# Performance work log

Hardware: AMD Instinct MI355X
Metric: run time of the kernel (lower is better)

The kernel has to match this reference:

```python
import jax, jax.numpy as jnp
import numpy as np
from jax import lax

# Module hyperparameters (init_kwargs)
B, T, F, H = 512, 256, 64, 128
D = F + H            # decoder LSTMCell width = input_dim + hidden_rnn
OUT_DIM = 32         # output_dim (survival horizon steps)
RISKS = 2
NEG = -1e10


def lstm_cell(x, h, c, Wih, Whh):
    # PyTorch gate order: i, f, g, o; bias=False
    g = x @ Wih.T + h @ Whh.T
    i, f, gg, o = jnp.split(g, 4, axis=-1)
    c = jax.nn.sigmoid(f) * c + jax.nn.sigmoid(i) * jnp.tanh(gg)
    h = jax.nn.sigmoid(o) * jnp.tanh(c)
    return h, c


def setup_inputs() -> dict:
    key = jax.random.key(0)
    ks = jax.random.split(key, 12)
    rn = lambda k, shp, fan: jax.random.normal(k, shp, jnp.float32) * (1.0 / np.sqrt(fan))
    return {
        "x": jax.random.normal(ks[0], (B, T, F), jnp.float32),
        # encoder LSTM (1 layer, bias=False)
        "W_ih_emb": rn(ks[1], (4 * H, F), F),
        "W_hh_emb": rn(ks[2], (4 * H, H), H),
        # longitudinal head: Linear(H -> F)
        "W_long": rn(ks[3], (F, H), H),
        "b_long": jnp.zeros((F,), jnp.float32),
        # attention head: Linear(F+H -> 1)
        "W_att": rn(ks[4], (1, D), D),
        "b_att": jnp.zeros((1,), jnp.float32),
        # per-risk cause-specific LSTMCell (bias=False) and Linear(D -> 1)
        "W_ih_cs": rn(ks[5], (RISKS, 4 * D, D), D),
        "W_hh_cs": rn(ks[6], (RISKS, 4 * D, D), D),
        "W_cs": rn(ks[7], (RISKS, 1, D), D),
        "b_cs": jnp.zeros((RISKS, 1), jnp.float32),
    }


def _forward(x, W_ih_emb, W_hh_emb, W_long, b_long, W_att, b_att,
             W_ih_cs, W_hh_cs, W_cs, b_cs):
    inputmask = jnp.abs(x).sum(2) == 0                      # [B,T]
    last_obs = (~inputmask).sum(axis=1) - 1                 # [B]

    # encoder LSTM over time
    def enc_step(carry, xt):
        h, c = carry
        h, c = lstm_cell(xt, h, c, W_ih_emb, W_hh_emb)
        return (h, c), h

    h0 = jnp.zeros((x.shape[0], H), x.dtype)
    _, hs = lax.scan(enc_step, (h0, h0), x.transpose(1, 0, 2))
    hidden = hs.transpose(1, 0, 2)                          # [B,T,H]

    long_pred = hidden @ W_long.T + b_long                  # [B,T,F]

    x_last = x[jnp.arange(x.shape[0]), last_obs]            # [B,F]
    concat = jnp.concatenate(
        [hidden, jnp.broadcast_to(x_last[:, None, :], (x.shape[0], x.shape[1], F))], -1)
    scores = (concat @ W_att.T + b_att)[..., 0]             # [B,T]

    idx = jnp.arange(x.shape[1])[None, :]
    scores = jnp.where(idx >= last_obs[:, None], NEG, scores)
    att = jax.nn.softmax(scores, axis=1)
    att = jnp.where((last_obs > 0)[:, None], att, 0.0)      # rows with last_obs==0 zeroed

    hidden_att = jnp.einsum('bt,bth->bh', att, hidden)      # [B,H]
    ha = jnp.concatenate([hidden_att, x_last], 1)           # [B,D]

    state0 = (lax.stop_gradient(ha), lax.stop_gradient(ha))  # .detach() on init state
    rs = jnp.arange(OUT_DIM * RISKS) % RISKS                # k-major, r-minor loop order

    def dec_step(carry, r):
        h, c = carry
        h, c = lstm_cell(ha, h, c, W_ih_cs[r], W_hh_cs[r])
        out = jax.nn.sigmoid(h @ W_cs[r].T + b_cs[r])       # [B,1]
        return (h, c), out

    _, outs = lax.scan(dec_step, state0, rs)                # [steps,B,1]
    outcomes = jax.nn.softmax(outs[..., 0].T, axis=-1)      # [B, OUT_DIM*RISKS]
    parts = tuple(outcomes[:, i * OUT_DIM:(i + 1) * OUT_DIM] for i in range(RISKS))
    return (long_pred,) + parts


def reference(x, W_ih_emb, W_hh_emb, W_long, b_long, W_att, b_att,
              W_ih_cs, W_hh_cs, W_cs, b_cs):
    return _forward(x, W_ih_emb, W_hh_emb, W_long, b_long, W_att, b_att,
                    W_ih_cs, W_hh_cs, W_cs, b_cs)
```

## Files before the change

kernel.cpp:

```cpp
#include <hip/hip_runtime.h>
#include <stdint.h>

#define DEV __device__ __forceinline__
typedef unsigned short u16; typedef unsigned int u32; typedef unsigned long long u64;
typedef __attribute__((ext_vector_type(8))) short s8v;
typedef __attribute__((ext_vector_type(4))) float f4v;

#define Bb 512
#define Tt 256
#define Ff 64
#define Hh 128
#define Dd 192

DEV u16 f2bf(float f){ u32 u = __builtin_bit_cast(u32, f); u32 r = (u + 0x7fffu + ((u>>16)&1u)) >> 16; return (u16)r; }
DEV float bf2f(u16 h){ u32 u = ((u32)h)<<16; return __builtin_bit_cast(float, u); }
DEV float sigm(float x){ return __builtin_amdgcn_rcpf(1.0f + __expf(-x)); }
DEV float tanhfast(float x){ return 1.0f - 2.0f*__builtin_amdgcn_rcpf(1.0f + __expf(2.0f*x)); }

DEV f4v mfma16(s8v a, s8v b, f4v c){ return __builtin_amdgcn_mfma_f32_16x16x32_bf16(a, b, c, 0, 0, 0); }

DEV void barrier_lds(){ asm volatile("s_waitcnt lgkmcnt(0)\n\ts_barrier" ::: "memory"); }

DEV int hxe(int k, int c){ int blk = k>>3; return (blk*16 + (c ^ ((blk&3)<<1)))*8 + (k&7); }

DEV s8v pack8(const float* p){
  const float4 a = *(const float4*)p; const float4 b = *(const float4*)(p+4);
  s8v r; r[0]=(short)f2bf(a.x); r[1]=(short)f2bf(a.y); r[2]=(short)f2bf(a.z); r[3]=(short)f2bf(a.w);
  r[4]=(short)f2bf(b.x); r[5]=(short)f2bf(b.y); r[6]=(short)f2bf(b.z); r[7]=(short)f2bf(b.w); return r;
}
DEV u32 pk2(float a, float b){ return (u32)f2bf(a) | ((u32)f2bf(b)<<16); }

__global__ __launch_bounds__(64) void prelim_k(const float* __restrict__ x,
    const float* __restrict__ Watt, const float* __restrict__ batt,
    float* __restrict__ xlast, float* __restrict__ c0, int* __restrict__ lastobs)
{
  int b = blockIdx.x, tid = threadIdx.x;
  int cnt = 0;
  for (int it = 0; it < 4; ++it){
    int t = it*64 + tid;
    const float4* p = (const float4*)(x + ((size_t)b*Tt + t)*Ff);
    float s = 0.0f;
    #pragma unroll
    for (int q = 0; q < 16; ++q){ float4 v = p[q]; s += fabsf(v.x)+fabsf(v.y)+fabsf(v.z)+fabsf(v.w); }
    u64 m = __ballot(s != 0.0f);
    cnt += __popcll(m);
  }
  int last = cnt - 1;
  int li = (last < 0) ? (Tt-1) : last;
  float xl = x[((size_t)b*Tt + li)*Ff + tid];
  xlast[b*Ff + tid] = xl;
  float p = xl * Watt[Hh + tid];
  for (int off = 32; off; off >>= 1) p += __shfl_down(p, off);
  if (tid == 0){ c0[b] = p + batt[0]; lastobs[b] = last; }
}

__global__ __launch_bounds__(256) void prep_wd_k(const float* __restrict__ Whhcs,
    const float* __restrict__ Wihcs, u16* __restrict__ Wd, u16* __restrict__ WdIH)
{
  int idx = blockIdx.x*256 + threadIdx.x;
  int j = idx & 7, lane = (idx>>3)&63;
  int f = idx>>9;
  int kt = f % 6; int mtr = f/6;
  int mt = mtr % 48, r = mtr/48;
  int ut = mt>>2, g = mt&3;
  int row = g*Dd + ut*16 + (lane&15);
  int k = kt*32 + (lane>>4)*8 + j;
  size_t src = ((size_t)r*768 + row)*Dd + k;
  Wd[idx]   = f2bf(Whhcs[src]);
  WdIH[idx] = f2bf(Wihcs[src]);
}

__global__ __launch_bounds__(64) void xw_k(const u16* __restrict__ WdIH,
    const float* __restrict__ ha, u16* __restrict__ xwg)
{
  int lane = threadIdx.x, l15 = lane&15, l4 = lane>>4;
  int cg = blockIdx.x & 3, rm = blockIdx.x >> 2;
  s8v af[6];
  #pragma unroll
  for (int kt=0;kt<6;++kt) af[kt] = *(const s8v*)(WdIH + (size_t)(rm*6+kt)*512 + lane*8);
  #pragma unroll
  for (int ct=0; ct<8; ++ct){
    int c = cg*128 + ct*16 + l15;
    f4v a = {0,0,0,0};
    #pragma unroll
    for (int kt=0;kt<6;++kt){
      s8v b = pack8(ha + (size_t)c*Dd + kt*32 + l4*8);
      a = mfma16(af[kt], b, a);
    }
    int bg = cg*8 + ct;
    int base = bg*24576 + rm*256 + l15*16 + l4*4;
    *(u32*)&xwg[base]   = pk2(a[0], a[1]);
    *(u32*)&xwg[base+2] = pk2(a[2], a[3]);
  }
}

__global__ __launch_bounds__(512,2) void enc_k(
    const float* __restrict__ x, const float* __restrict__ Whh, const float* __restrict__ Wih,
    const float* __restrict__ Wlong, const float* __restrict__ blong, const float* __restrict__ Watt,
    const float* __restrict__ xlast, const float* __restrict__ c0v, const int* __restrict__ lastobs,
    float* __restrict__ lp_out, float* __restrict__ ha)
{
  __shared__ __align__(16) u16 hx[2][3072];
  __shared__ float lp_lds[2][16*68];
  __shared__ float sarr[2][16];
  const int tid = threadIdx.x, wid = tid>>6, lane = tid&63, l15 = lane&15, l4 = lane>>4;
  const int b0 = blockIdx.x*16;
  const int xrow = tid>>5, xc2 = (tid&31)*2;

  s8v wf[4][6];
  #pragma unroll
  for (int mt = 0; mt < 4; ++mt){
    int gate = mt*Hh + wid*16 + l15;
    #pragma unroll
    for (int kt = 0; kt < 6; ++kt){
      int k0 = kt*32 + l4*8;
      if (kt < 4) wf[mt][kt] = pack8(Whh + (size_t)gate*Hh + k0);
      else        wf[mt][kt] = pack8(Wih + (size_t)gate*Ff + (k0 - Hh));
    }
  }
  s8v wfx[6];
  {
    s8v z = {0,0,0,0,0,0,0,0};
    #pragma unroll
    for (int kt = 0; kt < 6; ++kt) wfx[kt] = z;
    if (wid < 4){
      int f = wid*16 + l15;
      #pragma unroll
      for (int kt = 0; kt < 4; ++kt) wfx[kt] = pack8(Wlong + (size_t)f*Hh + kt*32 + l4*8);
    } else if (wid == 4 && l15 == 0){
      #pragma unroll
      for (int kt = 0; kt < 4; ++kt) wfx[kt] = pack8(Watt + kt*32 + l4*8);
    }
  }
  float bl[4] = {0,0,0,0};
  if (wid < 4){
    #pragma unroll
    for (int j = 0; j < 4; ++j) bl[j] = blong[wid*16 + l4*4 + j];
  }
  const int   lastb = lastobs[b0 + l15];
  const float c0b   = c0v[b0 + l15];

  const int he0 = hxe(wid*16 + l4*4, l15);
  const int xe0 = hxe(Hh + xc2, xrow);

  ((u64*)hx[0])[tid] = 0ull;
  {
    float2 xv = *(const float2*)(x + ((size_t)(b0+xrow)*Tt + 0)*Ff + xc2);
    *(u32*)&hx[0][xe0] = pk2(xv.x, xv.y);
  }
  float2 xa[4], xb[4];
  #pragma unroll
  for (int u = 0; u < 4; ++u)
    xa[u] = *(const float2*)(x + ((size_t)(b0+xrow)*Tt + (1+u))*Ff + xc2);
  __syncthreads();

  float cst[4] = {0,0,0,0}, hp[4] = {0,0,0,0}, hpp[4] = {0,0,0,0};
  float accA[4] = {0,0,0,0}, mrun = -3.0e38f, zrun = 0.0f;

  for (int tb = 0; tb < Tt; tb += 4){
    #pragma unroll
    for (int u = 0; u < 4; ++u){
      int tp = tb + 5 + u; if (tp > Tt-1) tp = Tt-1;
      xb[u] = *(const float2*)(x + ((size_t)(b0+xrow)*Tt + tp)*Ff + xc2);
    }
    #pragma unroll
    for (int u = 0; u < 4; ++u){
      const int t = tb + u;
      const int curb = u & 1, nxtb = curb ^ 1;
      s8v bf[6];
      #pragma unroll
      for (int kt = 0; kt < 6; ++kt)
        bf[kt] = *(const s8v*)&hx[curb][((kt*4 + l4)*16 + (l15 ^ (l4<<1)))*8];

      f4v acc0 = {0,0,0,0}, acc1 = {0,0,0,0}, acc2 = {0,0,0,0}, acc3 = {0,0,0,0}, accx = {0,0,0,0};
      #pragma unroll
      for (int kt = 0; kt < 6; ++kt){
        acc0 = mfma16(wf[0][kt], bf[kt], acc0);
        acc1 = mfma16(wf[1][kt], bf[kt], acc1);
        acc2 = mfma16(wf[2][kt], bf[kt], acc2);
        acc3 = mfma16(wf[3][kt], bf[kt], acc3);
      }
      if (wid < 5){
        #pragma unroll
        for (int kt = 0; kt < 6; ++kt) accx = mfma16(wfx[kt], bf[kt], accx);
      }
      if (wid == 4 && l4 == 0) sarr[nxtb][l15] = accx[0] + c0b;

      float hnew[4];
      #pragma unroll
      for (int j = 0; j < 4; ++j){
        float cn = sigm(acc1[j])*cst[j] + sigm(acc0[j])*tanhfast(acc2[j]);
        cst[j] = cn;
        hnew[j] = sigm(acc3[j])*tanhfast(cn);
      }
      if (t >= 2){
        float sv = sarr[curb][l15];
        if (t-2 < lastb){
          float mn = fmaxf(mrun, sv);
          float sc = __expf(mrun - mn);
          float e  = __expf(sv - mn);
          zrun = zrun*sc + e;
          #pragma unroll
          for (int j = 0; j < 4; ++j) accA[j] = accA[j]*sc + e*hpp[j];
          mrun = mn;
        }
      }
      #pragma unroll
      for (int j = 0; j < 4; ++j){ hpp[j] = hp[j]; hp[j] = hnew[j]; }
      {
        u64 w = (u64)pk2(hnew[0],hnew[1]) | ((u64)pk2(hnew[2],hnew[3])<<32);
        *(u64*)&hx[nxtb][he0] = w;
      }
      if (t < Tt-1) *(u32*)&hx[nxtb][xe0] = pk2(xa[u].x, xa[u].y);
      if (wid < 4){
        #pragma unroll
        for (int j = 0; j < 4; ++j)
          lp_lds[nxtb][l15*68 + wid*16 + l4*4 + j] = accx[j] + bl[j];
      }
      if (t >= 2){
        float2 v; v.x = lp_lds[curb][xrow*68 + xc2]; v.y = lp_lds[curb][xrow*68 + xc2 + 1];
        *(float2*)(lp_out + ((size_t)(b0+xrow)*Tt + (t-2))*Ff + xc2) = v;
      }
      barrier_lds();
    }
    #pragma unroll
    for (int u = 0; u < 4; ++u) xa[u] = xb[u];
  }
  {
    if (254 < lastb){
      float sv = sarr[0][l15];
      float mn = fmaxf(mrun, sv);
      float sc = __expf(mrun - mn);
      float e  = __expf(sv - mn);
      zrun = zrun*sc + e;
      #pragma unroll
      for (int j = 0; j < 4; ++j) accA[j] = accA[j]*sc + e*hpp[j];
      mrun = mn;
    }
    { float2 v; v.x = lp_lds[0][xrow*68 + xc2]; v.y = lp_lds[0][xrow*68 + xc2 + 1];
      *(float2*)(lp_out + ((size_t)(b0+xrow)*Tt + 254)*Ff + xc2) = v; }
    s8v bfE[4];
    #pragma unroll
    for (int kt = 0; kt < 4; ++kt)
      bfE[kt] = *(const s8v*)&hx[0][((kt*4 + l4)*16 + (l15 ^ (l4<<1)))*8];
    if (wid < 4){
      f4v accx = {0,0,0,0};
      #pragma unroll
      for (int kt = 0; kt < 4; ++kt) accx = mfma16(wfx[kt], bfE[kt], accx);
      #pragma unroll
      for (int j = 0; j < 4; ++j) lp_lds[1][l15*68 + wid*16 + l4*4 + j] = accx[j] + bl[j];
    }
    float inv = (zrun > 0.0f) ? __builtin_amdgcn_rcpf(zrun) : 0.0f;
    #pragma unroll
    for (int j = 0; j < 4; ++j)
      ha[(size_t)(b0 + l15)*Dd + wid*16 + l4*4 + j] = accA[j]*inv;
    __syncthreads();
    { float2 v; v.x = lp_lds[1][xrow*68 + xc2]; v.y = lp_lds[1][xrow*68 + xc2 + 1];
      *(float2*)(lp_out + ((size_t)(b0+xrow)*Tt + 255)*Ff + xc2) = v; }
    for (int q = tid; q < 16*Ff; q += 512){
      int r2 = q >> 6, f = q & 63;
      ha[(size_t)(b0 + r2)*Dd + Hh + f] = xlast[(b0 + r2)*Ff + f];
    }
  }
}

__global__ __launch_bounds__(256,1) void dec_k(const float* __restrict__ ha,
    const u16* __restrict__ Wd, const u16* __restrict__ xwg,
    const float* __restrict__ Wcs, const float* __restrict__ bcs, float* __restrict__ outs)
{
  __shared__ __align__(16) u16 hx[2][3072];
  __shared__ __align__(16) u16 w1[48*2*512];
  __shared__ __align__(16) u16 xwl[2*48*256];
  __shared__ float red[2][4][16];
  const int tid = threadIdx.x, wid = tid>>6, lane = tid&63, l15 = lane&15, l4 = lane>>4;
  const int b0 = blockIdx.x*16;

  #pragma unroll
  for (int it = 0; it < 3; ++it){
    int k = it*64 + (tid>>4)*4, c = tid&15;
    float4 v = *(const float4*)(ha + (size_t)(b0+c)*Dd + k);
    int e = hxe(k, c);
    *(u32*)&hx[0][e]   = pk2(v.x, v.y);
    *(u32*)&hx[0][e+2] = pk2(v.z, v.w);
  }
  {
    const u16* src = xwg + (size_t)blockIdx.x*24576;
    #pragma unroll
    for (int i = 0; i < 12; ++i){
      int off = (i*256 + tid)*8;
      *(s8v*)&xwl[off] = *(const s8v*)(src + off);
    }
  }
  #pragma unroll
  for (int i = 0; i < 24; ++i){
    int off = (i*256 + tid)*8;
    int chunk = off>>9, inner = off&511;
    int mtg = chunk>>1, kt = chunk&1;
    *(s8v*)&w1[off] = *(const s8v*)(Wd + (size_t)((48+mtg)*6+kt)*512 + inner);
  }
  s8v wreg[12][6];
  #pragma unroll
  for (int m = 0; m < 12; ++m)
    #pragma unroll
    for (int kt = 0; kt < 6; ++kt)
      wreg[m][kt] = *(const s8v*)(Wd + (size_t)((wid*12+m)*6+kt)*512 + lane*8);

  float cst[3][4], wcsr0[3][4], wcsr1[3][4];
  #pragma unroll
  for (int ut = 0; ut < 3; ++ut){
    int u0 = (wid*3+ut)*16 + l4*4;
    #pragma unroll
    for (int jj = 0; jj < 4; ++jj){
      cst[ut][jj]   = ha[(size_t)(b0+l15)*Dd + u0 + jj];
      wcsr0[ut][jj] = Wcs[u0 + jj];
      wcsr1[ut][jj] = Wcs[Dd + u0 + jj];
    }
  }
  const float bc0 = bcs[0], bc1 = bcs[1];
  __syncthreads();

  const u16* wsb = Wd + (size_t)(48 + wid*12)*6*512 + lane*8;
  s8v st[3][4];
#define LOADS(sl_, m_) { _Pragma("unroll") for (int q=0;q<4;++q) st[sl_][q] = *(const s8v*)(wsb + (size_t)((m_)*6 + 2 + q)*512); }

#define XWINIT(r_, m_, a_) { \
    int xb_ = ((r_)*48 + wid*12 + (m_))*256 + l15*16 + l4*4; \
    u32 q0 = *(const u32*)&xwl[xb_]; u32 q1 = *(const u32*)&xwl[xb_+2]; \
    a_[0] = bf2f((u16)q0); a_[1] = bf2f((u16)(q0>>16)); \
    a_[2] = bf2f((u16)q1); a_[3] = bf2f((u16)(q1>>16)); }

#define CELLS(r_, ut_, wcs_, a0_, a1_, a2_, a3_) { \
    float hn0,hn1,hn2,hn3; \
    { float cn = sigm(a1_[0])*cst[ut_][0] + sigm(a0_[0])*tanhfast(a2_[0]); cst[ut_][0]=cn; hn0 = sigm(a3_[0])*tanhfast(cn); } \
    { float cn = sigm(a1_[1])*cst[ut_][1] + sigm(a0_[1])*tanhfast(a2_[1]); cst[ut_][1]=cn; hn1 = sigm(a3_[1])*tanhfast(cn); } \
    { float cn = sigm(a1_[2])*cst[ut_][2] + sigm(a0_[2])*tanhfast(a2_[2]); cst[ut_][2]=cn; hn2 = sigm(a3_[2])*tanhfast(cn); } \
    { float cn = sigm(a1_[3])*cst[ut_][3] + sigm(a0_[3])*tanhfast(a2_[3]); cst[ut_][3]=cn; hn3 = sigm(a3_[3])*tanhfast(cn); } \
    part += hn0*wcs_[ut_][0] + hn1*wcs_[ut_][1] + hn2*wcs_[ut_][2] + hn3*wcs_[ut_][3]; \
    int u0_ = (wid*3+(ut_))*16 + l4*4; \
    int e0_ = (((u0_>>3)*16) + (l15 ^ (((u0_>>3)&3)<<1)))*8 + (u0_&7); \
    u64 w_ = (u64)pk2(hn0,hn1) | ((u64)pk2(hn2,hn3)<<32); \
    *(u64*)&hx[nxtb_][e0_] = w_; }

  for (int sp = 0; sp < 32; ++sp){
    {
      LOADS(0, 0); LOADS(1, 1); LOADS(2, 2);
      const int nxtb_ = 1;
      s8v bf[6];
      #pragma unroll
      for (int kt = 0; kt < 6; ++kt)
        bf[kt] = *(const s8v*)&hx[0][((kt*4 + l4)*16 + (l15 ^ (l4<<1)))*8];
      float part = 0.0f;
      #pragma unroll
      for (int ut = 0; ut < 3; ++ut){
        f4v a0,a1,a2,a3;
        XWINIT(0, ut*4+0, a0); XWINIT(0, ut*4+1, a1); XWINIT(0, ut*4+2, a2); XWINIT(0, ut*4+3, a3);
        #pragma unroll
        for (int kt = 0; kt < 6; ++kt){
          a0 = mfma16(wreg[ut*4+0][kt], bf[kt], a0);
          a1 = mfma16(wreg[ut*4+1][kt], bf[kt], a1);
          a2 = mfma16(wreg[ut*4+2][kt], bf[kt], a2);
          a3 = mfma16(wreg[ut*4+3][kt], bf[kt], a3);
        }
        CELLS(0, ut, wcsr0, a0, a1, a2, a3);
      }
      part += __shfl_xor(part, 16); part += __shfl_xor(part, 32);
      if (l4 == 0) red[0][wid][l15] = part;
      barrier_lds();
      if (tid < 16)
        outs[(sp*2)*Bb + b0 + tid] = sigm(red[0][0][tid]+red[0][1][tid]+red[0][2][tid]+red[0][3][tid] + bc0);
    }
    {
      const int nxtb_ = 0;
      s8v bf[6];
      #pragma unroll
      for (int kt = 0; kt < 6; ++kt)
        bf[kt] = *(const s8v*)&hx[1][((kt*4 + l4)*16 + (l15 ^ (l4<<1)))*8];
      float part = 0.0f;
      #pragma unroll
      for (int ut = 0; ut < 3; ++ut){
        f4v a0,a1,a2,a3;
        XWINIT(1, ut*4+0, a0); XWINIT(1, ut*4+1, a1); XWINIT(1, ut*4+2, a2); XWINIT(1, ut*4+3, a3);
        #pragma unroll
        for (int g = 0; g < 4; ++g){
          const int m = ut*4 + g;
          const int sl = m % 3;
          f4v* ap = (g==0)? &a0 : (g==1)? &a1 : (g==2)? &a2 : &a3;
          f4v a = *ap;
          { s8v w0 = *(const s8v*)&w1[((wid*12+m)*2+0)*512 + lane*8];
            s8v w1v= *(const s8v*)&w1[((wid*12+m)*2+1)*512 + lane*8];
            a = mfma16(w0, bf[0], a); a = mfma16(w1v, bf[1], a); }
          a = mfma16(st[sl][0], bf[2], a); a = mfma16(st[sl][1], bf[3], a);
          a = mfma16(st[sl][2], bf[4], a); a = mfma16(st[sl][3], bf[5], a);
          if (m+3 < 12) LOADS(sl, m+3);
          *ap = a;
        }
        CELLS(1, ut, wcsr1, a0, a1, a2, a3);
      }
      part += __shfl_xor(part, 16); part += __shfl_xor(part, 32);
      if (l4 == 0) red[1][wid][l15] = part;
      barrier_lds();
      if (tid < 16)
        outs[(sp*2+1)*Bb + b0 + tid] = sigm(red[1][0][tid]+red[1][1][tid]+red[1][2][tid]+red[1][3][tid] + bc1);
    }
  }
#undef LOADS
#undef XWINIT
#undef CELLS
}

__global__ __launch_bounds__(256) void fin_k(const float* __restrict__ outs, float* __restrict__ dout)
{
  int row = blockIdx.x*256 + threadIdx.x;
  float v[64]; float mx = -3.0e38f;
  #pragma unroll
  for (int s = 0; s < 64; ++s){ v[s] = outs[s*Bb + row]; mx = fmaxf(mx, v[s]); }
  float sum = 0.0f;
  #pragma unroll
  for (int s = 0; s < 64; ++s){ v[s] = __expf(v[s] - mx); sum += v[s]; }
  float inv = __builtin_amdgcn_rcpf(sum);
  float* p0 = dout + (size_t)Bb*Tt*Ff;
  float* p1 = p0 + Bb*32;
  #pragma unroll
  for (int j = 0; j < 32; ++j) p0[row*32 + j] = v[j]*inv;
  #pragma unroll
  for (int j = 0; j < 32; ++j) p1[row*32 + j] = v[32 + j]*inv;
}

extern "C" void kernel_launch(void* const* d_in, const int* in_sizes, int n_in,
                              void* d_out, int out_size, void* d_ws, size_t ws_size,
                              hipStream_t stream)
{
  const float* x      = (const float*)d_in[0];
  const float* Wih    = (const float*)d_in[1];
  const float* Whh    = (const float*)d_in[2];
  const float* Wlong  = (const float*)d_in[3];
  const float* blong  = (const float*)d_in[4];
  const float* Watt   = (const float*)d_in[5];
  const float* batt   = (const float*)d_in[6];
  const float* Wihcs  = (const float*)d_in[7];
  const float* Whhcs  = (const float*)d_in[8];
  const float* Wcs    = (const float*)d_in[9];
  const float* bcs    = (const float*)d_in[10];
  float* out = (float*)d_out;
  char* ws = (char*)d_ws;

  float* xlast   = (float*)ws;
  float* c0      = (float*)(ws + 131072);
  int*   lastobs = (int*)  (ws + 133120);
  float* ha      = (float*)(ws + 135168);
  u16*   Wd      = (u16*)  (ws + 528384);
  u16*   WdIH    = (u16*)  (ws + 1118208);
  u16*   xwg     = (u16*)  (ws + 1708032);
  float* outs    = (float*)(ws + 3280896);

  prep_wd_k<<<1152, 256, 0, stream>>>(Whhcs, Wihcs, Wd, WdIH);
  prelim_k<<<Bb, 64, 0, stream>>>(x, Watt, batt, xlast, c0, lastobs);
  enc_k<<<32, 512, 0, stream>>>(x, Whh, Wih, Wlong, blong, Watt, xlast, c0, lastobs, out, ha);
  xw_k<<<384, 64, 0, stream>>>(WdIH, ha, xwg);
  dec_k<<<32, 256, 0, stream>>>(ha, Wd, xwg, Wcs, bcs, outs);
  fin_k<<<2, 256, 0, stream>>>(outs, out);
}
```

Before: 583.8 us.

## Fold log2e into LSTM weights, use exp2 gates, restructure encoder and decoder loops

Pre-scales the gate weights by log2(e) (2*log2(e) for the g gate) so the sigmoid and tanh activations can use exp2 directly without an extra multiply. It also switches bf16 packing to the hardware v_cvt_pk_bf16_f32 instruction and rewrites the encoder loop as a two-step unrolled macro with a single-step x prefetch. The second-risk decoder step now loads its weight stream per unit tile in 4-gate groups with interleaved MFMAs, and the xw unpack uses 64-bit loads. This aims to cut VALU work in the serial recurrence, at the cost of changing rounding and of the rounding mode of the packing instruction.

```diff
diff --git a/kernel.cpp b/kernel.cpp
--- a/kernel.cpp
+++ b/kernel.cpp
@@ -11,11 +11,15 @@
 #define Ff 64
 #define Hh 128
 #define Dd 192
+#define L2E  1.4426950408889634f
+#define L2E2 2.8853900817779268f
 
 DEV u16 f2bf(float f){ u32 u = __builtin_bit_cast(u32, f); u32 r = (u + 0x7fffu + ((u>>16)&1u)) >> 16; return (u16)r; }
 DEV float bf2f(u16 h){ u32 u = ((u32)h)<<16; return __builtin_bit_cast(float, u); }
 DEV float sigm(float x){ return __builtin_amdgcn_rcpf(1.0f + __expf(-x)); }
-DEV float tanhfast(float x){ return 1.0f - 2.0f*__builtin_amdgcn_rcpf(1.0f + __expf(2.0f*x)); }
+DEV float sig2(float y){ return __builtin_amdgcn_rcpf(1.0f + exp2f(-y)); }
+DEV float th2 (float y){ return 1.0f - 2.0f*__builtin_amdgcn_rcpf(1.0f + exp2f(y)); }
+DEV u32 cvtpk(float lo, float hi){ u32 d; asm("v_cvt_pk_bf16_f32 %0, %1, %2" : "=v"(d) : "v"(lo), "v"(hi)); return d; }
 
 DEV f4v mfma16(s8v a, s8v b, f4v c){ return __builtin_amdgcn_mfma_f32_16x16x32_bf16(a, b, c, 0, 0, 0); }
 
@@ -23,11 +27,12 @@
 
 DEV int hxe(int k, int c){ int blk = k>>3; return (blk*16 + (c ^ ((blk&3)<<1)))*8 + (k&7); }
 
-DEV s8v pack8(const float* p){
+DEV s8v pack8s(const float* p, float sc){
   const float4 a = *(const float4*)p; const float4 b = *(const float4*)(p+4);
-  s8v r; r[0]=(short)f2bf(a.x); r[1]=(short)f2bf(a.y); r[2]=(short)f2bf(a.z); r[3]=(short)f2bf(a.w);
-  r[4]=(short)f2bf(b.x); r[5]=(short)f2bf(b.y); r[6]=(short)f2bf(b.z); r[7]=(short)f2bf(b.w); return r;
-}
+  s8v r; r[0]=(short)f2bf(a.x*sc); r[1]=(short)f2bf(a.y*sc); r[2]=(short)f2bf(a.z*sc); r[3]=(short)f2bf(a.w*sc);
+  r[4]=(short)f2bf(b.x*sc); r[5]=(short)f2bf(b.y*sc); r[6]=(short)f2bf(b.z*sc); r[7]=(short)f2bf(b.w*sc); return r;
+}
+DEV s8v pack8(const float* p){ return pack8s(p, 1.0f); }
 DEV u32 pk2(float a, float b){ return (u32)f2bf(a) | ((u32)f2bf(b)<<16); }
 
 __global__ __launch_bounds__(64) void prelim_k(const float* __restrict__ x,
@@ -65,9 +70,10 @@
   int ut = mt>>2, g = mt&3;
   int row = g*Dd + ut*16 + (lane&15);
   int k = kt*32 + (lane>>4)*8 + j;
+  float sc = (g == 2) ? L2E2 : L2E;
   size_t src = ((size_t)r*768 + row)*Dd + k;
-  Wd[idx]   = f2bf(Whhcs[src]);
-  WdIH[idx] = f2bf(Wihcs[src]);
+  Wd[idx]   = f2bf(Whhcs[src] * sc);
+  WdIH[idx] = f2bf(Wihcs[src] * sc);
 }
 
 __global__ __launch_bounds__(64) void xw_k(const u16* __restrict__ WdIH,
@@ -111,11 +117,12 @@
   #pragma unroll
   for (int mt = 0; mt < 4; ++mt){
     int gate = mt*Hh + wid*16 + l15;
+    float sc = (mt == 2) ? L2E2 : L2E;
     #pragma unroll
     for (int kt = 0; kt < 6; ++kt){
       int k0 = kt*32 + l4*8;
-      if (kt < 4) wf[mt][kt] = pack8(Whh + (size_t)gate*Hh + k0);
-      else        wf[mt][kt] = pack8(Wih + (size_t)gate*Ff + (k0 - Hh));
+      if (kt < 4) wf[mt][kt] = pack8s(Whh + (size_t)gate*Hh + k0, sc);
+      else        wf[mt][kt] = pack8s(Wih + (size_t)gate*Ff + (k0 - Hh), sc);
     }
   }
   s8v wfx[6];
@@ -146,86 +153,79 @@
   ((u64*)hx[0])[tid] = 0ull;
   {
     float2 xv = *(const float2*)(x + ((size_t)(b0+xrow)*Tt + 0)*Ff + xc2);
-    *(u32*)&hx[0][xe0] = pk2(xv.x, xv.y);
-  }
-  float2 xa[4], xb[4];
-  #pragma unroll
-  for (int u = 0; u < 4; ++u)
-    xa[u] = *(const float2*)(x + ((size_t)(b0+xrow)*Tt + (1+u))*Ff + xc2);
+    *(u32*)&hx[0][xe0] = cvtpk(xv.x, xv.y);
+  }
+  float2 xa = *(const float2*)(x + ((size_t)(b0+xrow)*Tt + 1)*Ff + xc2);
+  float2 xb;
   __syncthreads();
 
   float cst[4] = {0,0,0,0}, hp[4] = {0,0,0,0}, hpp[4] = {0,0,0,0};
   float accA[4] = {0,0,0,0}, mrun = -3.0e38f, zrun = 0.0f;
 
-  for (int tb = 0; tb < Tt; tb += 4){
-    #pragma unroll
-    for (int u = 0; u < 4; ++u){
-      int tp = tb + 5 + u; if (tp > Tt-1) tp = Tt-1;
-      xb[u] = *(const float2*)(x + ((size_t)(b0+xrow)*Tt + tp)*Ff + xc2);
-    }
-    #pragma unroll
-    for (int u = 0; u < 4; ++u){
-      const int t = tb + u;
-      const int curb = u & 1, nxtb = curb ^ 1;
-      s8v bf[6];
-      #pragma unroll
-      for (int kt = 0; kt < 6; ++kt)
-        bf[kt] = *(const s8v*)&hx[curb][((kt*4 + l4)*16 + (l15 ^ (l4<<1)))*8];
-
-      f4v acc0 = {0,0,0,0}, acc1 = {0,0,0,0}, acc2 = {0,0,0,0}, acc3 = {0,0,0,0}, accx = {0,0,0,0};
-      #pragma unroll
-      for (int kt = 0; kt < 6; ++kt){
-        acc0 = mfma16(wf[0][kt], bf[kt], acc0);
-        acc1 = mfma16(wf[1][kt], bf[kt], acc1);
-        acc2 = mfma16(wf[2][kt], bf[kt], acc2);
-        acc3 = mfma16(wf[3][kt], bf[kt], acc3);
-      }
-      if (wid < 5){
-        #pragma unroll
-        for (int kt = 0; kt < 6; ++kt) accx = mfma16(wfx[kt], bf[kt], accx);
-      }
-      if (wid == 4 && l4 == 0) sarr[nxtb][l15] = accx[0] + c0b;
-
-      float hnew[4];
-      #pragma unroll
-      for (int j = 0; j < 4; ++j){
-        float cn = sigm(acc1[j])*cst[j] + sigm(acc0[j])*tanhfast(acc2[j]);
-        cst[j] = cn;
-        hnew[j] = sigm(acc3[j])*tanhfast(cn);
-      }
-      if (t >= 2){
-        float sv = sarr[curb][l15];
-        if (t-2 < lastb){
-          float mn = fmaxf(mrun, sv);
-          float sc = __expf(mrun - mn);
-          float e  = __expf(sv - mn);
-          zrun = zrun*sc + e;
-          #pragma unroll
-          for (int j = 0; j < 4; ++j) accA[j] = accA[j]*sc + e*hpp[j];
-          mrun = mn;
-        }
-      }
-      #pragma unroll
-      for (int j = 0; j < 4; ++j){ hpp[j] = hp[j]; hp[j] = hnew[j]; }
-      {
-        u64 w = (u64)pk2(hnew[0],hnew[1]) | ((u64)pk2(hnew[2],hnew[3])<<32);
-        *(u64*)&hx[nxtb][he0] = w;
-      }
-      if (t < Tt-1) *(u32*)&hx[nxtb][xe0] = pk2(xa[u].x, xa[u].y);
-      if (wid < 4){
-        #pragma unroll
-        for (int j = 0; j < 4; ++j)
-          lp_lds[nxtb][l15*68 + wid*16 + l4*4 + j] = accx[j] + bl[j];
-      }
-      if (t >= 2){
-        float2 v; v.x = lp_lds[curb][xrow*68 + xc2]; v.y = lp_lds[curb][xrow*68 + xc2 + 1];
-        *(float2*)(lp_out + ((size_t)(b0+xrow)*Tt + (t-2))*Ff + xc2) = v;
-      }
-      barrier_lds();
-    }
-    #pragma unroll
-    for (int u = 0; u < 4; ++u) xa[u] = xb[u];
-  }
+#define ENC_STEP(T_, CURB_, NXTB_, XC_, XN_) { \
+    const int t = (T_); \
+    s8v bf[6]; \
+    _Pragma("unroll") \
+    for (int kt = 0; kt < 6; ++kt) \
+      bf[kt] = *(const s8v*)&hx[CURB_][((kt*4 + l4)*16 + (l15 ^ (l4<<1)))*8]; \
+    { int tp = t + 2; if (tp > Tt-1) tp = Tt-1; \
+      XN_ = *(const float2*)(x + ((size_t)(b0+xrow)*Tt + tp)*Ff + xc2); } \
+    f4v acc0 = {0,0,0,0}, acc1 = {0,0,0,0}, acc2 = {0,0,0,0}, acc3 = {0,0,0,0}, accx = {0,0,0,0}; \
+    _Pragma("unroll") \
+    for (int kt = 0; kt < 6; ++kt){ \
+      acc0 = mfma16(wf[0][kt], bf[kt], acc0); \
+      acc1 = mfma16(wf[1][kt], bf[kt], acc1); \
+      acc2 = mfma16(wf[2][kt], bf[kt], acc2); \
+      acc3 = mfma16(wf[3][kt], bf[kt], acc3); \
+    } \
+    if (wid < 5){ \
+      _Pragma("unroll") \
+      for (int kt = 0; kt < 6; ++kt) accx = mfma16(wfx[kt], bf[kt], accx); \
+    } \
+    if (wid == 4 && l4 == 0) sarr[NXTB_][l15] = accx[0] + c0b; \
+    float hnew[4]; \
+    _Pragma("unroll") \
+    for (int j = 0; j < 4; ++j){ \
+      float si = sig2(acc0[j]), sf = sig2(acc1[j]); \
+      float tg = th2(acc2[j]),  so = sig2(acc3[j]); \
+      float cn = sf*cst[j] + si*tg; \
+      cst[j] = cn; \
+      hnew[j] = so * th2(cn * L2E2); \
+    } \
+    if (t >= 2){ \
+      float sv = sarr[CURB_][l15]; \
+      if (t-2 < lastb){ \
+        float mn = fmaxf(mrun, sv); \
+        float sc = __expf(mrun - mn); \
+        float e  = __expf(sv - mn); \
+        zrun = zrun*sc + e; \
+        _Pragma("unroll") \
+        for (int j = 0; j < 4; ++j) accA[j] = accA[j]*sc + e*hpp[j]; \
+        mrun = mn; \
+      } \
+    } \
+    _Pragma("unroll") \
+    for (int j = 0; j < 4; ++j){ hpp[j] = hp[j]; hp[j] = hnew[j]; } \
+    { u32 plo = cvtpk(hnew[0], hnew[1]), phi = cvtpk(hnew[2], hnew[3]); \
+      *(u64*)&hx[NXTB_][he0] = (u64)plo | ((u64)phi<<32); } \
+    if (t < Tt-1) *(u32*)&hx[NXTB_][xe0] = cvtpk(XC_.x, XC_.y); \
+    if (wid < 4){ \
+      _Pragma("unroll") \
+      for (int j = 0; j < 4; ++j) \
+        lp_lds[NXTB_][l15*68 + wid*16 + l4*4 + j] = accx[j] + bl[j]; \
+    } \
+    if (t >= 2){ \
+      float2 v; v.x = lp_lds[CURB_][xrow*68 + xc2]; v.y = lp_lds[CURB_][xrow*68 + xc2 + 1]; \
+      *(float2*)(lp_out + ((size_t)(b0+xrow)*Tt + (t-2))*Ff + xc2) = v; \
+    } \
+    barrier_lds(); }
+
+  for (int tp2 = 0; tp2 < 128; ++tp2){
+    ENC_STEP(2*tp2,   0, 1, xa, xb)
+    ENC_STEP(2*tp2+1, 1, 0, xb, xa)
+  }
+#undef ENC_STEP
+
   {
     if (254 < lastb){
       float sv = sarr[0][l15];
@@ -280,8 +280,8 @@
     int k = it*64 + (tid>>4)*4, c = tid&15;
     float4 v = *(const float4*)(ha + (size_t)(b0+c)*Dd + k);
     int e = hxe(k, c);
-    *(u32*)&hx[0][e]   = pk2(v.x, v.y);
-    *(u32*)&hx[0][e+2] = pk2(v.z, v.w);
+    *(u32*)&hx[0][e]   = cvtpk(v.x, v.y);
+    *(u32*)&hx[0][e+2] = cvtpk(v.z, v.w);
   }
   {
     const u16* src = xwg + (size_t)blockIdx.x*24576;
@@ -320,31 +320,37 @@
   __syncthreads();
 
   const u16* wsb = Wd + (size_t)(48 + wid*12)*6*512 + lane*8;
-  s8v st[3][4];
-#define LOADS(sl_, m_) { _Pragma("unroll") for (int q=0;q<4;++q) st[sl_][q] = *(const s8v*)(wsb + (size_t)((m_)*6 + 2 + q)*512); }
+  s8v st[4][4];
+#define LOADS_UT(ut_) { \
+    _Pragma("unroll") for (int g_=0; g_<4; ++g_) \
+      _Pragma("unroll") for (int q_=0; q_<4; ++q_) \
+        st[g_][q_] = *(const s8v*)(wsb + (size_t)(((ut_)*4+g_)*6 + 2 + q_)*512); }
 
 #define XWINIT(r_, m_, a_) { \
     int xb_ = ((r_)*48 + wid*12 + (m_))*256 + l15*16 + l4*4; \
-    u32 q0 = *(const u32*)&xwl[xb_]; u32 q1 = *(const u32*)&xwl[xb_+2]; \
-    a_[0] = bf2f((u16)q0); a_[1] = bf2f((u16)(q0>>16)); \
-    a_[2] = bf2f((u16)q1); a_[3] = bf2f((u16)(q1>>16)); }
-
-#define CELLS(r_, ut_, wcs_, a0_, a1_, a2_, a3_) { \
-    float hn0,hn1,hn2,hn3; \
-    { float cn = sigm(a1_[0])*cst[ut_][0] + sigm(a0_[0])*tanhfast(a2_[0]); cst[ut_][0]=cn; hn0 = sigm(a3_[0])*tanhfast(cn); } \
-    { float cn = sigm(a1_[1])*cst[ut_][1] + sigm(a0_[1])*tanhfast(a2_[1]); cst[ut_][1]=cn; hn1 = sigm(a3_[1])*tanhfast(cn); } \
-    { float cn = sigm(a1_[2])*cst[ut_][2] + sigm(a0_[2])*tanhfast(a2_[2]); cst[ut_][2]=cn; hn2 = sigm(a3_[2])*tanhfast(cn); } \
-    { float cn = sigm(a1_[3])*cst[ut_][3] + sigm(a0_[3])*tanhfast(a2_[3]); cst[ut_][3]=cn; hn3 = sigm(a3_[3])*tanhfast(cn); } \
-    part += hn0*wcs_[ut_][0] + hn1*wcs_[ut_][1] + hn2*wcs_[ut_][2] + hn3*wcs_[ut_][3]; \
+    u64 q_ = *(const u64*)&xwl[xb_]; \
+    u32 qlo_ = (u32)q_, qhi_ = (u32)(q_>>32); \
+    a_[0] = __builtin_bit_cast(float, qlo_<<16); \
+    a_[1] = __builtin_bit_cast(float, qlo_ & 0xffff0000u); \
+    a_[2] = __builtin_bit_cast(float, qhi_<<16); \
+    a_[3] = __builtin_bit_cast(float, qhi_ & 0xffff0000u); }
+
+#define CELLS(ut_, wcs_, nxtb_, a0_, a1_, a2_, a3_) { \
+    float hn[4]; \
+    _Pragma("unroll") for (int j = 0; j < 4; ++j){ \
+      float si = sig2(a0_[j]), sf = sig2(a1_[j]); \
+      float tg = th2(a2_[j]),  so = sig2(a3_[j]); \
+      float cn = sf*cst[ut_][j] + si*tg; \
+      cst[ut_][j] = cn; \
+      hn[j] = so * th2(cn * L2E2); \
+      part += hn[j] * wcs_[ut_][j]; } \
+    u32 plo_ = cvtpk(hn[0], hn[1]), phi_ = cvtpk(hn[2], hn[3]); \
     int u0_ = (wid*3+(ut_))*16 + l4*4; \
     int e0_ = (((u0_>>3)*16) + (l15 ^ (((u0_>>3)&3)<<1)))*8 + (u0_&7); \
-    u64 w_ = (u64)pk2(hn0,hn1) | ((u64)pk2(hn2,hn3)<<32); \
-    *(u64*)&hx[nxtb_][e0_] = w_; }
+    *(u64*)&hx[nxtb_][e0_] = (u64)plo_ | ((u64)phi_<<32); }
 
   for (int sp = 0; sp < 32; ++sp){
     {
-      LOADS(0, 0); LOADS(1, 1); LOADS(2, 2);
-      const int nxtb_ = 1;
       s8v bf[6];
       #pragma unroll
       for (int kt = 0; kt < 6; ++kt)
@@ -361,8 +367,9 @@
           a2 = mfma16(wreg[ut*4+2][kt], bf[kt], a2);
           a3 = mfma16(wreg[ut*4+3][kt], bf[kt], a3);
         }
-        CELLS(0, ut, wcsr0, a0, a1, a2, a3);
+        CELLS(ut, wcsr0, 1, a0, a1, a2, a3);
       }
+      LOADS_UT(0);
       part += __shfl_xor(part, 16); part += __shfl_xor(part, 32);
       if (l4 == 0) red[0][wid][l15] = part;
       barrier_lds();
@@ -370,7 +377,6 @@
         outs[(sp*2)*Bb + b0 + tid] = sigm(red[0][0][tid]+red[0][1][tid]+red[0][2][tid]+red[0][3][tid] + bc0);
     }
     {
-      const int nxtb_ = 0;
       s8v bf[6];
       #pragma unroll
       for (int kt = 0; kt < 6; ++kt)
@@ -381,20 +387,25 @@
         f4v a0,a1,a2,a3;
         XWINIT(1, ut*4+0, a0); XWINIT(1, ut*4+1, a1); XWINIT(1, ut*4+2, a2); XWINIT(1, ut*4+3, a3);
         #pragma unroll
-        for (int g = 0; g < 4; ++g){
-          const int m = ut*4 + g;
-          const int sl = m % 3;
-          f4v* ap = (g==0)? &a0 : (g==1)? &a1 : (g==2)? &a2 : &a3;
-          f4v a = *ap;
-          { s8v w0 = *(const s8v*)&w1[((wid*12+m)*2+0)*512 + lane*8];
-            s8v w1v= *(const s8v*)&w1[((wid*12+m)*2+1)*512 + lane*8];
-            a = mfma16(w0, bf[0], a); a = mfma16(w1v, bf[1], a); }
-          a = mfma16(st[sl][0], bf[2], a); a = mfma16(st[sl][1], bf[3], a);
-          a = mfma16(st[sl][2], bf[4], a); a = mfma16(st[sl][3], bf[5], a);
-          if (m+3 < 12) LOADS(sl, m+3);
-          *ap = a;
+        for (int kt = 0; kt < 2; ++kt){
+          s8v q0 = *(const s8v*)&w1[((wid*12+ut*4+0)*2+kt)*512 + lane*8];
+          s8v q1 = *(const s8v*)&w1[((wid*12+ut*4+1)*2+kt)*512 + lane*8];
+          s8v q2 = *(const s8v*)&w1[((wid*12+ut*4+2)*2+kt)*512 + lane*8];
+          s8v q3 = *(const s8v*)&w1[((wid*12+ut*4+3)*2+kt)*512 + lane*8];
+          a0 = mfma16(q0, bf[kt], a0);
+          a1 = mfma16(q1, bf[kt], a1);
+          a2 = mfma16(q2, bf[kt], a2);
+          a3 = mfma16(q3, bf[kt], a3);
         }
-        CELLS(1, ut, wcsr1, a0, a1, a2, a3);
+        #pragma unroll
+        for (int q = 0; q < 4; ++q){
+          a0 = mfma16(st[0][q], bf[2+q], a0);
+          a1 = mfma16(st[1][q], bf[2+q], a1);
+          a2 = mfma16(st[2][q], bf[2+q], a2);
+          a3 = mfma16(st[3][q], bf[2+q], a3);
+        }
+        if (ut < 2) LOADS_UT(ut+1);
+        CELLS(ut, wcsr1, 0, a0, a1, a2, a3);
       }
       part += __shfl_xor(part, 16); part += __shfl_xor(part, 32);
       if (l4 == 0) red[1][wid][l15] = part;
@@ -403,7 +414,7 @@
         outs[(sp*2+1)*Bb + b0 + tid] = sigm(red[1][0][tid]+red[1][1][tid]+red[1][2][tid]+red[1][3][tid] + bc1);
     }
   }
-#undef LOADS
+#undef LOADS_UT
 #undef XWINIT
 #undef CELLS
 }
```

New measurement: 671.8 us. +15.1%, slower.
